# Kernel tuning notes

Measured on AMD Instinct MI355X. Metric: run time of the kernel, lower is better.

The kernel has to match this reference:

```python
import jax, jax.numpy as jnp
import numpy as np

B, C, H, W = 4, 256, 64, 64
NHEAD = 8
KH = KW = 3          # partition = [3, 3] -> 9-token windows, stride 1, padding 1
EPS = 1e-5           # torch LayerNorm default


def setup_inputs() -> dict:
    key = jax.random.key(0)
    ks = jax.random.split(key, 3)
    s = 1.0 / np.sqrt(C)  # xavier-ish scale
    return {
        "src": jax.random.normal(ks[0], (B, C, H, W), jnp.float32),
        "ln_w": jnp.ones((C,), jnp.float32),
        "ln_b": jnp.zeros((C,), jnp.float32),
        "in_proj_w": jax.random.normal(ks[1], (3 * C, C), jnp.float32) * s,
        "in_proj_b": jnp.zeros((3 * C,), jnp.float32),
        "out_proj_w": jax.random.normal(ks[2], (C, C), jnp.float32) * s,
        "out_proj_b": jnp.zeros((C,), jnp.float32),
    }


def reference(src, ln_w, ln_b, in_proj_w, in_proj_b, out_proj_w, out_proj_b):
    b, c, h, w = src.shape
    L = h * w
    S = KH * KW  # 9 tokens per local window
    # --- Unfold: overlapping 3x3 windows, padding 1, stride 1 (torch.nn.Unfold order: c major, kernel pos minor)
    xp = jnp.pad(src, ((0, 0), (0, 0), (1, 1), (1, 1)))
    patches = jnp.stack(
        [xp[:, :, i : i + h, j : j + w] for i in range(KH) for j in range(KW)], axis=2
    )  # [b, c, 9, h, w]
    x = patches.reshape(b, c, S, L).transpose(2, 0, 3, 1).reshape(S, b * L, c)  # [S, bL, c]
    # --- Pre-norm (norm1); note: pos embed in the source is overwritten (q = k = src2), FFN is dead code
    mu = x.mean(-1, keepdims=True)
    var = ((x - mu) ** 2).mean(-1, keepdims=True)
    x2 = (x - mu) / jnp.sqrt(var + EPS) * ln_w + ln_b
    # --- MultiheadAttention (self-attn, eval mode -> no dropout)
    qkv = jnp.einsum("sbc,dc->sbd", x2, in_proj_w) + in_proj_b  # [S, bL, 3c]
    q, k, v = jnp.split(qkv, 3, axis=-1)
    dh = c // NHEAD
    scale = dh ** -0.5
    q = q.reshape(S, b * L, NHEAD, dh) * scale
    k = k.reshape(S, b * L, NHEAD, dh)
    v = v.reshape(S, b * L, NHEAD, dh)
    scores = jnp.einsum("sbhd,tbhd->bhst", q, k)        # [bL, H, 9, 9]
    attn = jax.nn.softmax(scores, axis=-1)
    o = jnp.einsum("bhst,tbhd->sbhd", attn, v).reshape(S, b * L, c)
    o = jnp.einsum("sbc,dc->sbd", o, out_proj_w) + out_proj_b
    y = x + o  # residual
    # --- Fold back (kernel 1x1, stride 1): each output pixel = its window's center token
    center = y[S // 2]  # [bL, c]
    return center.reshape(b, L, c).transpose(0, 2, 1).reshape(b, c, h, w)
```

## Files before the change

### kernel.cpp

```cpp
#include <hip/hip_runtime.h>
#include <math.h>


#define NPIX 16384
#define HW   4096
#define CDIM 256

typedef short  bf16x8 __attribute__((ext_vector_type(8)));
typedef float  f32x4  __attribute__((ext_vector_type(4)));
typedef unsigned short u16x8 __attribute__((ext_vector_type(8)));
typedef unsigned short u16x4 __attribute__((ext_vector_type(4)));

__device__ inline float bf2f(unsigned short u) {
    unsigned v = ((unsigned)u) << 16;
    return __builtin_bit_cast(float, v);
}
__device__ inline unsigned short f2bf(float f) {
    unsigned u = __builtin_bit_cast(unsigned, f);
    u += 0x7FFFu + ((u >> 16) & 1u);
    return (unsigned short)(u >> 16);
}
__device__ inline void sb0() { __builtin_amdgcn_sched_barrier(0); }

__global__ __launch_bounds__(256) void k_prep(const float* __restrict__ Wqkv,
                                              const float* __restrict__ Wout,
                                              const float* __restrict__ bqkv,
                                              const float* __restrict__ lnb,
                                              unsigned short* __restrict__ Wqkvbf,
                                              unsigned short* __restrict__ Woutbf,
                                              float* __restrict__ pads) {
    int bid = blockIdx.x, t = threadIdx.x;
    if (bid < 192) {
        int i = bid * 256 + t;
        float4 v = ((const float4*)Wqkv)[i];
        u16x4 o = { f2bf(v.x), f2bf(v.y), f2bf(v.z), f2bf(v.w) };
        *(u16x4*)(Wqkvbf + i * 4) = o;
    } else if (bid < 256) {
        int i = (bid - 192) * 256 + t;
        float4 v = ((const float4*)Wout)[i];
        u16x4 o = { f2bf(v.x), f2bf(v.y), f2bf(v.z), f2bf(v.w) };
        *(u16x4*)(Woutbf + i * 4) = o;
    } else {
        int tg = (bid - 256) * 256 + t;
        int d = tg >> 4, part = tg & 15;
        int row = 256 + d;
        const float* wr = Wqkv + (size_t)row * CDIM + part * 16;
        float s = 0.f;
        #pragma unroll
        for (int c = 0; c < 16; ++c) s += lnb[part * 16 + c] * wr[c];
        s += __shfl_xor(s, 1);
        s += __shfl_xor(s, 2);
        s += __shfl_xor(s, 4);
        s += __shfl_xor(s, 8);
        if (part == 0) pads[d] = s + bqkv[row];
    }
}

__device__ inline void stage32(const unsigned short* __restrict__ g, int grow0,
                               int koff, unsigned short* dst, int lane) {
    int r16  = lane >> 2;
    int slot = lane & 3;
    #pragma unroll
    for (int it = 0; it < 4; ++it) {
        int row = it * 16 + r16;
        const unsigned short* src = g + (size_t)(grow0 + row) * 256 + koff
                                      + ((slot ^ ((row >> 1) & 3)) * 8);
        __builtin_amdgcn_global_load_lds(
            (const __attribute__((address_space(1))) void*)src,
            (__attribute__((address_space(3))) void*)(dst + it * 16 * 32),
            16, 0, 0);
    }
}

__global__ __launch_bounds__(256, 3) void k_ln_qkv(const float* __restrict__ src,
                                                   const float* __restrict__ lnw,
                                                   const float* __restrict__ lnb,
                                                   const unsigned short* __restrict__ Wbf,
                                                   const float* __restrict__ bias,
                                                   unsigned short* __restrict__ qkvbf) {
    __shared__ unsigned short As[32 * 256];
    __shared__ unsigned short Bs[4 * 4096];
    __shared__ float redS[8 * 33 * 2 + 64];

    int t = threadIdx.x;
    int bid = blockIdx.x;
    int sb = (bid & 7) * 64 + (bid >> 3);
    int n0 = sb * 32;
    int b = n0 >> 12, p0 = n0 & 4095;
    int lane = t & 63, wv = t >> 6;
    int lr = lane & 15, lg = lane >> 4;
    unsigned short* BsW = Bs + wv * 4096;

    stage32(Wbf, wv * 64, 0, BsW, lane);

    float bj[3][4];
    #pragma unroll
    for (int p = 0; p < 3; ++p)
        #pragma unroll
        for (int j = 0; j < 4; ++j)
            bj[p][j] = bias[p * 256 + wv * 64 + j * 16 + lr];

    {
        float* red  = redS;
        float* red2 = redS + 264;
        float* muv  = redS + 528;
        float* rsv  = redS + 560;
        int pix = t & 31, q = t >> 5;
        const float* sp = src + ((size_t)b * CDIM) * HW + p0 + pix;
        float x[32];
        float sum = 0.f, sq = 0.f;
        #pragma unroll
        for (int i = 0; i < 32; ++i) {
            x[i] = sp[(size_t)(q * 32 + i) * HW];
            sum += x[i]; sq += x[i] * x[i];
        }
        red[q * 33 + pix] = sum; red2[q * 33 + pix] = sq;
        __syncthreads();
        if (t < 32) {
            float s = 0.f, s2 = 0.f;
            #pragma unroll
            for (int qq = 0; qq < 8; ++qq) { s += red[qq * 33 + t]; s2 += red2[qq * 33 + t]; }
            float mu = s * (1.f / 256.f);
            float var = fmaxf(s2 * (1.f / 256.f) - mu * mu, 0.f);
            muv[t] = mu; rsv[t] = rsqrtf(var + 1e-5f);
        }
        __syncthreads();
        float mu = muv[pix], rs = rsv[pix];
        #pragma unroll
        for (int c8 = 0; c8 < 4; ++c8) {
            u16x8 o8;
            #pragma unroll
            for (int j = 0; j < 8; ++j) {
                int c = q * 32 + c8 * 8 + j;
                float xn = (x[c8 * 8 + j] - mu) * rs * lnw[c] + lnb[c];
                o8[j] = f2bf(xn);
            }
            int chunk = q * 4 + c8;
            *(u16x8*)((char*)As + (pix * 512 + (((chunk & 7) ^ (pix & 7)) | (chunk & 24)) * 16)) = o8;
        }
    }
    __syncthreads();

    for (int pass = 0; pass < 3; ++pass) {
        int d0 = pass * 256;
        f32x4 acc[2][4] = {};
        #pragma unroll
        for (int kc = 0; kc < 8; ++kc) {
            sb0();
            if (kc < 7) {
                stage32(Wbf, d0 + wv * 64, (kc + 1) * 32,
                        BsW + ((kc + 1) & 1) * 2048, lane);
                asm volatile("s_waitcnt vmcnt(4)" ::: "memory");
            } else if (pass < 2) {
                stage32(Wbf, (pass + 1) * 256 + wv * 64, 0, BsW, lane);
                asm volatile("s_waitcnt vmcnt(4)" ::: "memory");
            } else {
                asm volatile("s_waitcnt vmcnt(0)" ::: "memory");
            }
            sb0();
            const unsigned short* B = BsW + (kc & 1) * 2048;
            int chA = kc * 4 + lg;
            bf16x8 a[2], bb[4];
            #pragma unroll
            for (int i = 0; i < 2; ++i) {
                int r = i * 16 + lr;
                int sl = ((chA & 7) ^ (r & 7)) | (chA & 24);
                a[i] = *(bf16x8*)((char*)As + (r * 512 + sl * 16));
            }
            #pragma unroll
            for (int j = 0; j < 4; ++j) {
                int rb = j * 16 + lr;
                int sl = lg ^ ((rb >> 1) & 3);
                bb[j] = *(bf16x8*)(B + rb * 32 + sl * 8);
            }
            __builtin_amdgcn_s_setprio(1);
            #pragma unroll
            for (int i = 0; i < 2; ++i)
                #pragma unroll
                for (int j = 0; j < 4; ++j)
                    acc[i][j] = __builtin_amdgcn_mfma_f32_16x16x32_bf16(
                        a[i], bb[j], acc[i][j], 0, 0, 0);
            __builtin_amdgcn_s_setprio(0);
        }
        sb0();
        unsigned short* Ct = BsW + 2048;
        #pragma unroll
        for (int j = 0; j < 4; ++j) {
            #pragma unroll
            for (int i = 0; i < 2; ++i)
                #pragma unroll
                for (int r2 = 0; r2 < 4; ++r2) {
                    int row = i * 16 + lg * 4 + r2;
                    int col = j * 16 + lr;
                    int ch  = col >> 3;
                    int sl  = ch ^ (row & 7);
                    Ct[row * 64 + sl * 8 + (col & 7)] = f2bf(acc[i][j][r2] + bj[pass][j]);
                }
        }
        #pragma unroll
        for (int it2 = 0; it2 < 4; ++it2) {
            int row = 8 * it2 + (lane >> 3);
            int chunk = lane & 7;
            int sl = chunk ^ (row & 7);
            bf16x8 v = *(bf16x8*)(Ct + row * 64 + sl * 8);
            *(bf16x8*)(qkvbf + (size_t)(n0 + row) * 768 + d0 + wv * 64 + chunk * 8) = v;
        }
    }
}

__global__ __launch_bounds__(256, 3) void k_attn_proj(const unsigned short* __restrict__ qkvbf,
                                                      const float* __restrict__ pads,
                                                      const unsigned short* __restrict__ Wbf,
                                                      const float* __restrict__ bias,
                                                      const float* __restrict__ src,
                                                      float* __restrict__ out) {
    __shared__ unsigned short Bt[32 * 264];
    __shared__ unsigned short Ws[4 * 4096];
    int t  = threadIdx.x;
    int bid = blockIdx.x;
    int sb  = (bid & 7) * 64 + (bid >> 3);
    int n0 = sb * 32;
    int b  = n0 >> 12;
    int p0 = n0 & 4095;
    int lane = t & 63, wv = t >> 6;
    int lr = lane & 15, lg = lane >> 4;
    unsigned short* WsW = Ws + wv * 4096;

    stage32(Wbf, wv * 64, 0, WsW, lane);

    float bd[4][4];
    #pragma unroll
    for (int i = 0; i < 4; ++i)
        #pragma unroll
        for (int r2 = 0; r2 < 4; ++r2)
            bd[i][r2] = bias[wv * 64 + i * 16 + lg * 4 + r2];

    {
        int pix = t >> 3, h = t & 7;
        int n = n0 + pix;
        int p = n & 4095, hh0 = p >> 6, ww0 = p & 63;
        const float scale = 0.1767766952966369f;

        float qv[32];
        const unsigned short* qp = qkvbf + (size_t)n * 768 + h * 32;
        #pragma unroll
        for (int c8 = 0; c8 < 4; ++c8) {
            bf16x8 v = *(const bf16x8*)(qp + c8 * 8);
            #pragma unroll
            for (int j = 0; j < 8; ++j) qv[c8 * 8 + j] = bf2f((unsigned short)v[j]) * scale;
        }
        float sc[9];
        #pragma unroll
        for (int t9 = 0; t9 < 9; ++t9) {
            int dy = t9 / 3 - 1, dx = t9 % 3 - 1;
            int hh = hh0 + dy, ww = ww0 + dx;
            bool ok = ((unsigned)hh < 64u) && ((unsigned)ww < 64u);
            float a = 0.f;
            if (ok) {
                const unsigned short* kp = qkvbf + (size_t)(n + dy * 64 + dx) * 768 + 256 + h * 32;
                #pragma unroll
                for (int c8 = 0; c8 < 4; ++c8) {
                    bf16x8 v = *(const bf16x8*)(kp + c8 * 8);
                    #pragma unroll
                    for (int j = 0; j < 8; ++j) a += qv[c8 * 8 + j] * bf2f((unsigned short)v[j]);
                }
            } else {
                const float* pk = pads + h * 32;
                #pragma unroll
                for (int j = 0; j < 32; ++j) a += qv[j] * pk[j];
            }
            sc[t9] = a;
        }
        float m = sc[0];
        #pragma unroll
        for (int t9 = 1; t9 < 9; ++t9) m = fmaxf(m, sc[t9]);
        float s = 0.f;
        #pragma unroll
        for (int t9 = 0; t9 < 9; ++t9) { sc[t9] = __expf(sc[t9] - m); s += sc[t9]; }
        float inv = 1.0f / s;

        float ov[32];
        #pragma unroll
        for (int j = 0; j < 32; ++j) ov[j] = 0.f;
        #pragma unroll
        for (int t9 = 0; t9 < 9; ++t9) {
            int dy = t9 / 3 - 1, dx = t9 % 3 - 1;
            int hh = hh0 + dy, ww = ww0 + dx;
            bool ok = ((unsigned)hh < 64u) && ((unsigned)ww < 64u);
            float w = sc[t9] * inv;
            if (ok) {
                const unsigned short* vp = qkvbf + (size_t)(n + dy * 64 + dx) * 768 + 512 + h * 32;
                #pragma unroll
                for (int c8 = 0; c8 < 4; ++c8) {
                    bf16x8 v = *(const bf16x8*)(vp + c8 * 8);
                    #pragma unroll
                    for (int j = 0; j < 8; ++j) ov[c8 * 8 + j] += w * bf2f((unsigned short)v[j]);
                }
            } else {
                const float* pv = pads + 256 + h * 32;
                #pragma unroll
                for (int j = 0; j < 32; ++j) ov[j] += w * pv[j];
            }
        }
        #pragma unroll
        for (int c8 = 0; c8 < 4; ++c8) {
            u16x8 o8;
            #pragma unroll
            for (int j = 0; j < 8; ++j) o8[j] = f2bf(ov[c8 * 8 + j]);
            *(u16x8*)(Bt + pix * 264 + h * 32 + c8 * 8) = o8;
        }
    }
    __syncthreads();

    f32x4 acc[4][2] = {};
    #pragma unroll
    for (int kc = 0; kc < 8; ++kc) {
        sb0();
        if (kc < 7) {
            stage32(Wbf, wv * 64, (kc + 1) * 32, WsW + ((kc + 1) & 1) * 2048, lane);
            asm volatile("s_waitcnt vmcnt(4)" ::: "memory");
        } else {
            asm volatile("s_waitcnt vmcnt(0)" ::: "memory");
        }
        sb0();
        const unsigned short* A = WsW + (kc & 1) * 2048;
        bf16x8 a[4], bb[2];
        #pragma unroll
        for (int i = 0; i < 4; ++i) {
            int ri = i * 16 + lr;
            int sl = lg ^ ((ri >> 1) & 3);
            a[i] = *(bf16x8*)(A + ri * 32 + sl * 8);
        }
        #pragma unroll
        for (int j = 0; j < 2; ++j)
            bb[j] = *(bf16x8*)(Bt + (j * 16 + lr) * 264 + kc * 32 + lg * 8);
        __builtin_amdgcn_s_setprio(1);
        #pragma unroll
        for (int i = 0; i < 4; ++i)
            #pragma unroll
            for (int j = 0; j < 2; ++j)
                acc[i][j] = __builtin_amdgcn_mfma_f32_16x16x32_bf16(
                    a[i], bb[j], acc[i][j], 0, 0, 0);
        __builtin_amdgcn_s_setprio(0);
    }
    #pragma unroll
    for (int i = 0; i < 4; ++i) {
        #pragma unroll
        for (int r2 = 0; r2 < 4; ++r2) {
            int dg = wv * 64 + i * 16 + lg * 4 + r2;
            #pragma unroll
            for (int j = 0; j < 2; ++j) {
                int ng = p0 + j * 16 + lr;
                size_t idx = ((size_t)(b * CDIM + dg)) * HW + ng;
                out[idx] = acc[i][j][r2] + bd[i][r2] + src[idx];
            }
        }
    }
}

extern "C" void kernel_launch(void* const* d_in, const int* in_sizes, int n_in,
                              void* d_out, int out_size, void* d_ws, size_t ws_size,
                              hipStream_t stream) {
    const float* src  = (const float*)d_in[0];
    const float* lnw  = (const float*)d_in[1];
    const float* lnb  = (const float*)d_in[2];
    const float* Wqkv = (const float*)d_in[3];
    const float* bqkv = (const float*)d_in[4];
    const float* Wout = (const float*)d_in[5];
    const float* bout = (const float*)d_in[6];
    float* out = (float*)d_out;

    unsigned short* qkvbf  = (unsigned short*)d_ws;
    unsigned short* Wqkvbf = qkvbf + (size_t)NPIX * 768;
    unsigned short* Woutbf = Wqkvbf + 768 * 256;
    float* pads = (float*)(Woutbf + 256 * 256);

    k_prep<<<288, 256, 0, stream>>>(Wqkv, Wout, bqkv, lnb, Wqkvbf, Woutbf, pads);
    k_ln_qkv<<<512, 256, 0, stream>>>(src, lnw, lnb, Wqkvbf, bqkv, qkvbf);
    k_attn_proj<<<512, 256, 0, stream>>>(qkvbf, pads, Woutbf, bout, src, out);
}
```

Measured before the change: 51.25 us.

## Fuse weight prep into LN+QKV kernel, converting fp32 weights to bf16 on the fly

Removes the separate k_prep launch. The QKV GEMM now reads fp32 Wqkv directly, converts it to bf16 with v_cvt_pk_bf16_f32 and stores it into a single-buffered LDS tile. The Wout conversion and the pads bias dot products move into spare waves of the LN+QKV kernel. This saves one kernel launch and the bf16 weight round-trip through memory. In exchange it drops the async global_load_lds double-buffer pipelining, doubles the global weight bytes each block reads, and lowers launch bounds occupancy from 3 to 2.

```diff
diff --git a/kernel.cpp b/kernel.cpp
--- a/kernel.cpp
+++ b/kernel.cpp
@@ -10,6 +10,7 @@
 typedef float  f32x4  __attribute__((ext_vector_type(4)));
 typedef unsigned short u16x8 __attribute__((ext_vector_type(8)));
 typedef unsigned short u16x4 __attribute__((ext_vector_type(4)));
+typedef unsigned int   u32x4 __attribute__((ext_vector_type(4)));
 
 __device__ inline float bf2f(unsigned short u) {
     unsigned v = ((unsigned)u) << 16;
@@ -21,39 +22,10 @@
     return (unsigned short)(u >> 16);
 }
 __device__ inline void sb0() { __builtin_amdgcn_sched_barrier(0); }
-
-__global__ __launch_bounds__(256) void k_prep(const float* __restrict__ Wqkv,
-                                              const float* __restrict__ Wout,
-                                              const float* __restrict__ bqkv,
-                                              const float* __restrict__ lnb,
-                                              unsigned short* __restrict__ Wqkvbf,
-                                              unsigned short* __restrict__ Woutbf,
-                                              float* __restrict__ pads) {
-    int bid = blockIdx.x, t = threadIdx.x;
-    if (bid < 192) {
-        int i = bid * 256 + t;
-        float4 v = ((const float4*)Wqkv)[i];
-        u16x4 o = { f2bf(v.x), f2bf(v.y), f2bf(v.z), f2bf(v.w) };
-        *(u16x4*)(Wqkvbf + i * 4) = o;
-    } else if (bid < 256) {
-        int i = (bid - 192) * 256 + t;
-        float4 v = ((const float4*)Wout)[i];
-        u16x4 o = { f2bf(v.x), f2bf(v.y), f2bf(v.z), f2bf(v.w) };
-        *(u16x4*)(Woutbf + i * 4) = o;
-    } else {
-        int tg = (bid - 256) * 256 + t;
-        int d = tg >> 4, part = tg & 15;
-        int row = 256 + d;
-        const float* wr = Wqkv + (size_t)row * CDIM + part * 16;
-        float s = 0.f;
-        #pragma unroll
-        for (int c = 0; c < 16; ++c) s += lnb[part * 16 + c] * wr[c];
-        s += __shfl_xor(s, 1);
-        s += __shfl_xor(s, 2);
-        s += __shfl_xor(s, 4);
-        s += __shfl_xor(s, 8);
-        if (part == 0) pads[d] = s + bqkv[row];
-    }
+__device__ inline unsigned cvtpk(float a, float b) {
+    unsigned r;
+    asm("v_cvt_pk_bf16_f32 %0, %1, %2" : "=v"(r) : "v"(a), "v"(b));
+    return r;
 }
 
 __device__ inline void stage32(const unsigned short* __restrict__ g, int grow0,
@@ -72,14 +44,17 @@
     }
 }
 
-__global__ __launch_bounds__(256, 3) void k_ln_qkv(const float* __restrict__ src,
+__global__ __launch_bounds__(256, 2) void k_ln_qkv(const float* __restrict__ src,
                                                    const float* __restrict__ lnw,
                                                    const float* __restrict__ lnb,
-                                                   const unsigned short* __restrict__ Wbf,
-                                                   const float* __restrict__ bias,
-                                                   unsigned short* __restrict__ qkvbf) {
+                                                   const float* __restrict__ Wqkv,
+                                                   const float* __restrict__ bqkv,
+                                                   const float* __restrict__ Wout,
+                                                   unsigned short* __restrict__ qkvbf,
+                                                   unsigned short* __restrict__ Woutbf,
+                                                   float* __restrict__ pads) {
     __shared__ unsigned short As[32 * 256];
-    __shared__ unsigned short Bs[4 * 4096];
+    __shared__ unsigned short Bs[4 * 2048];
     __shared__ float redS[8 * 33 * 2 + 64];
 
     int t = threadIdx.x;
@@ -89,16 +64,14 @@
     int b = n0 >> 12, p0 = n0 & 4095;
     int lane = t & 63, wv = t >> 6;
     int lr = lane & 15, lg = lane >> 4;
-    unsigned short* BsW = Bs + wv * 4096;
-
-    stage32(Wbf, wv * 64, 0, BsW, lane);
+    unsigned short* BsW = Bs + wv * 2048;
 
     float bj[3][4];
     #pragma unroll
     for (int p = 0; p < 3; ++p)
         #pragma unroll
         for (int j = 0; j < 4; ++j)
-            bj[p][j] = bias[p * 256 + wv * 64 + j * 16 + lr];
+            bj[p][j] = bqkv[p * 256 + wv * 64 + j * 16 + lr];
 
     {
         float* red  = redS;
@@ -141,24 +114,41 @@
     }
     __syncthreads();
 
+    if (wv == 2 && lane < 32) {
+        int i = bid * 32 + lane;
+        float4 v = ((const float4*)Wout)[i];
+        u16x4 o = { f2bf(v.x), f2bf(v.y), f2bf(v.z), f2bf(v.w) };
+        *(u16x4*)(Woutbf + i * 4) = o;
+    }
+    if (wv == 3) {
+        int row = 256 + bid;
+        float4 w4 = *(const float4*)(Wqkv + (size_t)row * 256 + lane * 4);
+        float4 l4 = *(const float4*)(lnb + lane * 4);
+        float s = w4.x * l4.x + w4.y * l4.y + w4.z * l4.z + w4.w * l4.w;
+        s += __shfl_xor(s, 1);  s += __shfl_xor(s, 2);  s += __shfl_xor(s, 4);
+        s += __shfl_xor(s, 8);  s += __shfl_xor(s, 16); s += __shfl_xor(s, 32);
+        if (lane == 0) pads[bid] = s + bqkv[row];
+    }
+
+    int rrow = lane >> 2;
+    int kp   = lane & 3;
     for (int pass = 0; pass < 3; ++pass) {
         int d0 = pass * 256;
         f32x4 acc[2][4] = {};
         #pragma unroll
         for (int kc = 0; kc < 8; ++kc) {
-            sb0();
-            if (kc < 7) {
-                stage32(Wbf, d0 + wv * 64, (kc + 1) * 32,
-                        BsW + ((kc + 1) & 1) * 2048, lane);
-                asm volatile("s_waitcnt vmcnt(4)" ::: "memory");
-            } else if (pass < 2) {
-                stage32(Wbf, (pass + 1) * 256 + wv * 64, 0, BsW, lane);
-                asm volatile("s_waitcnt vmcnt(4)" ::: "memory");
-            } else {
-                asm volatile("s_waitcnt vmcnt(0)" ::: "memory");
-            }
-            sb0();
-            const unsigned short* B = BsW + (kc & 1) * 2048;
+            #pragma unroll
+            for (int it = 0; it < 4; ++it) {
+                int r = it * 16 + rrow;
+                const float* gp = Wqkv + (size_t)(d0 + wv * 64 + r) * 256
+                                       + kc * 32 + kp * 8;
+                float4 v0 = *(const float4*)gp;
+                float4 v1 = *(const float4*)(gp + 4);
+                u32x4 o = { cvtpk(v0.x, v0.y), cvtpk(v0.z, v0.w),
+                            cvtpk(v1.x, v1.y), cvtpk(v1.z, v1.w) };
+                int slot = kp ^ ((r >> 1) & 3);
+                *(u32x4*)(BsW + r * 32 + slot * 8) = o;
+            }
             int chA = kc * 4 + lg;
             bf16x8 a[2], bb[4];
             #pragma unroll
@@ -171,19 +161,16 @@
             for (int j = 0; j < 4; ++j) {
                 int rb = j * 16 + lr;
                 int sl = lg ^ ((rb >> 1) & 3);
-                bb[j] = *(bf16x8*)(B + rb * 32 + sl * 8);
-            }
-            __builtin_amdgcn_s_setprio(1);
+                bb[j] = *(bf16x8*)(BsW + rb * 32 + sl * 8);
+            }
             #pragma unroll
             for (int i = 0; i < 2; ++i)
                 #pragma unroll
                 for (int j = 0; j < 4; ++j)
                     acc[i][j] = __builtin_amdgcn_mfma_f32_16x16x32_bf16(
                         a[i], bb[j], acc[i][j], 0, 0, 0);
-            __builtin_amdgcn_s_setprio(0);
-        }
-        sb0();
-        unsigned short* Ct = BsW + 2048;
+        }
+        unsigned short* Ct = BsW;
         #pragma unroll
         for (int j = 0; j < 4; ++j) {
             #pragma unroll
@@ -371,11 +358,10 @@
     float* out = (float*)d_out;
 
     unsigned short* qkvbf  = (unsigned short*)d_ws;
-    unsigned short* Wqkvbf = qkvbf + (size_t)NPIX * 768;
-    unsigned short* Woutbf = Wqkvbf + 768 * 256;
+    unsigned short* Woutbf = qkvbf + (size_t)NPIX * 768;
     float* pads = (float*)(Woutbf + 256 * 256);
 
-    k_prep<<<288, 256, 0, stream>>>(Wqkv, Wout, bqkv, lnb, Wqkvbf, Woutbf, pads);
-    k_ln_qkv<<<512, 256, 0, stream>>>(src, lnw, lnb, Wqkvbf, bqkv, qkvbf);
+    k_ln_qkv<<<512, 256, 0, stream>>>(src, lnw, lnb, Wqkv, bqkv, Wout,
+                                      qkvbf, Woutbf, pads);
     k_attn_proj<<<512, 256, 0, stream>>>(qkvbf, pads, Woutbf, bout, src, out);
 }
```

After: 64.79 us. 1.26x slower.

## Use 8 waves per block in LN+QKV kernel with triple-buffered weight staging

Applied to the files above, without the earlier changes.

The LayerNorm+QKV GEMM kernel now runs with 512 threads (8 waves), each wave owning 32 output columns instead of 64. Weight tiles are staged into a 3-slot ring buffer two k-steps ahead across pass boundaries, replacing the previous double buffer. The aim is more waves to hide memory latency and deeper prefetch. The cost is fewer MFMAs per wave per load and the same A-tile LDS reads duplicated across more waves.

```diff
diff --git a/kernel.cpp b/kernel.cpp
--- a/kernel.cpp
+++ b/kernel.cpp
@@ -56,6 +56,160 @@
     }
 }
 
+__device__ inline void stage32x32(const unsigned short* __restrict__ g, int grow0,
+                                  int koff, unsigned short* dst, int lane) {
+    int rin  = lane >> 2;
+    int slot = lane & 3;
+    #pragma unroll
+    for (int it = 0; it < 2; ++it) {
+        int row = it * 16 + rin;
+        const unsigned short* src = g + (size_t)(grow0 + row) * 256 + koff
+                                      + ((slot ^ ((row >> 1) & 3)) * 8);
+        __builtin_amdgcn_global_load_lds(
+            (const __attribute__((address_space(1))) void*)src,
+            (__attribute__((address_space(3))) void*)(dst + it * 512),
+            16, 0, 0);
+    }
+}
+
+__global__ __launch_bounds__(512, 4) void k_ln_qkv(const float* __restrict__ src,
+                                                   const float* __restrict__ lnw,
+                                                   const float* __restrict__ lnb,
+                                                   const unsigned short* __restrict__ Wbf,
+                                                   const float* __restrict__ bias,
+                                                   unsigned short* __restrict__ qkvbf) {
+    __shared__ unsigned short As[32 * 256];
+    __shared__ unsigned short Ws[8 * 3 * 1024];
+    __shared__ float redS[16 * 33 * 2 + 64];
+
+    int t = threadIdx.x;
+    int bid = blockIdx.x;
+    int sb = (bid & 7) * 64 + (bid >> 3);
+    int n0 = sb * 32;
+    int b = n0 >> 12, p0 = n0 & 4095;
+    int lane = t & 63, wv = t >> 6;
+    int lr = lane & 15, lg = lane >> 4;
+    unsigned short* WsW = Ws + wv * 3072;
+
+    stage32x32(Wbf, wv * 32, 0, WsW, lane);
+    stage32x32(Wbf, wv * 32, 32, WsW + 1024, lane);
+
+    float bj[3][2];
+    #pragma unroll
+    for (int p = 0; p < 3; ++p)
+        #pragma unroll
+        for (int j = 0; j < 2; ++j)
+            bj[p][j] = bias[p * 256 + wv * 32 + j * 16 + lr];
+
+    {
+        float* red  = redS;
+        float* red2 = redS + 528;
+        float* muv  = redS + 1056;
+        float* rsv  = redS + 1088;
+        int pix = t & 31, q = t >> 5;
+        const float* sp = src + ((size_t)b * CDIM) * HW + p0 + pix;
+        float x[16];
+        float sum = 0.f, sq = 0.f;
+        #pragma unroll
+        for (int i = 0; i < 16; ++i) {
+            x[i] = sp[(size_t)(q * 16 + i) * HW];
+            sum += x[i]; sq += x[i] * x[i];
+        }
+        red[q * 33 + pix] = sum; red2[q * 33 + pix] = sq;
+        __syncthreads();
+        if (t < 32) {
+            float s = 0.f, s2 = 0.f;
+            #pragma unroll
+            for (int qq = 0; qq < 16; ++qq) { s += red[qq * 33 + t]; s2 += red2[qq * 33 + t]; }
+            float mu = s * (1.f / 256.f);
+            float var = fmaxf(s2 * (1.f / 256.f) - mu * mu, 0.f);
+            muv[t] = mu; rsv[t] = rsqrtf(var + 1e-5f);
+        }
+        __syncthreads();
+        float mu = muv[pix], rs = rsv[pix];
+        #pragma unroll
+        for (int c8 = 0; c8 < 2; ++c8) {
+            u16x8 o8;
+            #pragma unroll
+            for (int j = 0; j < 8; ++j) {
+                int c = q * 16 + c8 * 8 + j;
+                float xn = (x[c8 * 8 + j] - mu) * rs * lnw[c] + lnb[c];
+                o8[j] = f2bf(xn);
+            }
+            int chunk = q * 2 + c8;
+            *(u16x8*)((char*)As + (pix * 512 + (((chunk & 7) ^ (pix & 7)) | (chunk & 24)) * 16)) = o8;
+        }
+    }
+    __syncthreads();
+
+    for (int pass = 0; pass < 3; ++pass) {
+        int d0 = pass * 256;
+        f32x4 acc[2][2] = {};
+        #pragma unroll
+        for (int kc = 0; kc < 8; ++kc) {
+            int g = pass * 8 + kc;
+            sb0();
+            if (g < 22) {
+                int ng = g + 2;
+                stage32x32(Wbf, (ng >> 3) * 256 + wv * 32, (ng & 7) * 32,
+                           WsW + (ng % 3) * 1024, lane);
+                asm volatile("s_waitcnt vmcnt(4)" ::: "memory");
+            } else if (g == 22) {
+                asm volatile("s_waitcnt vmcnt(2)" ::: "memory");
+            } else {
+                asm volatile("s_waitcnt vmcnt(0)" ::: "memory");
+            }
+            sb0();
+            const unsigned short* B = WsW + (g % 3) * 1024;
+            int chA = kc * 4 + lg;
+            bf16x8 a[2], bb[2];
+            #pragma unroll
+            for (int i = 0; i < 2; ++i) {
+                int r = i * 16 + lr;
+                int sl = ((chA & 7) ^ (r & 7)) | (chA & 24);
+                a[i] = *(bf16x8*)((char*)As + (r * 512 + sl * 16));
+            }
+            #pragma unroll
+            for (int j = 0; j < 2; ++j) {
+                int rb = j * 16 + lr;
+                int sl = lg ^ ((rb >> 1) & 3);
+                bb[j] = *(bf16x8*)(B + rb * 32 + sl * 8);
+            }
+            __builtin_amdgcn_s_setprio(1);
+            #pragma unroll
+            for (int i = 0; i < 2; ++i)
+                #pragma unroll
+                for (int j = 0; j < 2; ++j)
+                    acc[i][j] = __builtin_amdgcn_mfma_f32_16x16x32_bf16(
+                        a[i], bb[j], acc[i][j], 0, 0, 0);
+            __builtin_amdgcn_s_setprio(0);
+        }
+        sb0();
+        unsigned short* Ct = WsW + ((pass * 8 + 7) % 3) * 1024;
+        #pragma unroll
+        for (int j = 0; j < 2; ++j) {
+            #pragma unroll
+            for (int i = 0; i < 2; ++i)
+                #pragma unroll
+                for (int r2 = 0; r2 < 4; ++r2) {
+                    int row = i * 16 + lg * 4 + r2;
+                    int col = j * 16 + lr;
+                    int ch  = col >> 3;
+                    int sl  = ch ^ ((row >> 1) & 3);
+                    Ct[row * 32 + sl * 8 + (col & 7)] = f2bf(acc[i][j][r2] + bj[pass][j]);
+                }
+        }
+        #pragma unroll
+        for (int it2 = 0; it2 < 2; ++it2) {
+            int row = it2 * 16 + (lane >> 2);
+            int chunk = lane & 3;
+            int sl = chunk ^ ((row >> 1) & 3);
+            bf16x8 v = *(bf16x8*)(Ct + row * 32 + sl * 8);
+            *(bf16x8*)(qkvbf + (size_t)(n0 + row) * 768 + d0 + wv * 32 + chunk * 8) = v;
+        }
+    }
+}
+
 __device__ inline void stage32(const unsigned short* __restrict__ g, int grow0,
                                int koff, unsigned short* dst, int lane) {
     int r16  = lane >> 2;
@@ -69,142 +223,6 @@
             (const __attribute__((address_space(1))) void*)src,
             (__attribute__((address_space(3))) void*)(dst + it * 16 * 32),
             16, 0, 0);
-    }
-}
-
-__global__ __launch_bounds__(256, 3) void k_ln_qkv(const float* __restrict__ src,
-                                                   const float* __restrict__ lnw,
-                                                   const float* __restrict__ lnb,
-                                                   const unsigned short* __restrict__ Wbf,
-                                                   const float* __restrict__ bias,
-                                                   unsigned short* __restrict__ qkvbf) {
-    __shared__ unsigned short As[32 * 256];
-    __shared__ unsigned short Bs[4 * 4096];
-    __shared__ float redS[8 * 33 * 2 + 64];
-
-    int t = threadIdx.x;
-    int bid = blockIdx.x;
-    int sb = (bid & 7) * 64 + (bid >> 3);
-    int n0 = sb * 32;
-    int b = n0 >> 12, p0 = n0 & 4095;
-    int lane = t & 63, wv = t >> 6;
-    int lr = lane & 15, lg = lane >> 4;
-    unsigned short* BsW = Bs + wv * 4096;
-
-    stage32(Wbf, wv * 64, 0, BsW, lane);
-
-    float bj[3][4];
-    #pragma unroll
-    for (int p = 0; p < 3; ++p)
-        #pragma unroll
-        for (int j = 0; j < 4; ++j)
-            bj[p][j] = bias[p * 256 + wv * 64 + j * 16 + lr];
-
-    {
-        float* red  = redS;
-        float* red2 = redS + 264;
-        float* muv  = redS + 528;
-        float* rsv  = redS + 560;
-        int pix = t & 31, q = t >> 5;
-        const float* sp = src + ((size_t)b * CDIM) * HW + p0 + pix;
-        float x[32];
-        float sum = 0.f, sq = 0.f;
-        #pragma unroll
-        for (int i = 0; i < 32; ++i) {
-            x[i] = sp[(size_t)(q * 32 + i) * HW];
-            sum += x[i]; sq += x[i] * x[i];
-        }
-        red[q * 33 + pix] = sum; red2[q * 33 + pix] = sq;
-        __syncthreads();
-        if (t < 32) {
-            float s = 0.f, s2 = 0.f;
-            #pragma unroll
-            for (int qq = 0; qq < 8; ++qq) { s += red[qq * 33 + t]; s2 += red2[qq * 33 + t]; }
-            float mu = s * (1.f / 256.f);
-            float var = fmaxf(s2 * (1.f / 256.f) - mu * mu, 0.f);
-            muv[t] = mu; rsv[t] = rsqrtf(var + 1e-5f);
-        }
-        __syncthreads();
-        float mu = muv[pix], rs = rsv[pix];
-        #pragma unroll
-        for (int c8 = 0; c8 < 4; ++c8) {
-            u16x8 o8;
-            #pragma unroll
-            for (int j = 0; j < 8; ++j) {
-                int c = q * 32 + c8 * 8 + j;
-                float xn = (x[c8 * 8 + j] - mu) * rs * lnw[c] + lnb[c];
-                o8[j] = f2bf(xn);
-            }
-            int chunk = q * 4 + c8;
-            *(u16x8*)((char*)As + (pix * 512 + (((chunk & 7) ^ (pix & 7)) | (chunk & 24)) * 16)) = o8;
-        }
-    }
-    __syncthreads();
-
-    for (int pass = 0; pass < 3; ++pass) {
-        int d0 = pass * 256;
-        f32x4 acc[2][4] = {};
-        #pragma unroll
-        for (int kc = 0; kc < 8; ++kc) {
-            sb0();
-            if (kc < 7) {
-                stage32(Wbf, d0 + wv * 64, (kc + 1) * 32,
-                        BsW + ((kc + 1) & 1) * 2048, lane);
-                asm volatile("s_waitcnt vmcnt(4)" ::: "memory");
-            } else if (pass < 2) {
-                stage32(Wbf, (pass + 1) * 256 + wv * 64, 0, BsW, lane);
-                asm volatile("s_waitcnt vmcnt(4)" ::: "memory");
-            } else {
-                asm volatile("s_waitcnt vmcnt(0)" ::: "memory");
-            }
-            sb0();
-            const unsigned short* B = BsW + (kc & 1) * 2048;
-            int chA = kc * 4 + lg;
-            bf16x8 a[2], bb[4];
-            #pragma unroll
-            for (int i = 0; i < 2; ++i) {
-                int r = i * 16 + lr;
-                int sl = ((chA & 7) ^ (r & 7)) | (chA & 24);
-                a[i] = *(bf16x8*)((char*)As + (r * 512 + sl * 16));
-            }
-            #pragma unroll
-            for (int j = 0; j < 4; ++j) {
-                int rb = j * 16 + lr;
-                int sl = lg ^ ((rb >> 1) & 3);
-                bb[j] = *(bf16x8*)(B + rb * 32 + sl * 8);
-            }
-            __builtin_amdgcn_s_setprio(1);
-            #pragma unroll
-            for (int i = 0; i < 2; ++i)
-                #pragma unroll
-                for (int j = 0; j < 4; ++j)
-                    acc[i][j] = __builtin_amdgcn_mfma_f32_16x16x32_bf16(
-                        a[i], bb[j], acc[i][j], 0, 0, 0);
-            __builtin_amdgcn_s_setprio(0);
-        }
-        sb0();
-        unsigned short* Ct = BsW + 2048;
-        #pragma unroll
-        for (int j = 0; j < 4; ++j) {
-            #pragma unroll
-            for (int i = 0; i < 2; ++i)
-                #pragma unroll
-                for (int r2 = 0; r2 < 4; ++r2) {
-                    int row = i * 16 + lg * 4 + r2;
-                    int col = j * 16 + lr;
-                    int ch  = col >> 3;
-                    int sl  = ch ^ (row & 7);
-                    Ct[row * 64 + sl * 8 + (col & 7)] = f2bf(acc[i][j][r2] + bj[pass][j]);
-                }
-        }
-        #pragma unroll
-        for (int it2 = 0; it2 < 4; ++it2) {
-            int row = 8 * it2 + (lane >> 3);
-            int chunk = lane & 7;
-            int sl = chunk ^ (row & 7);
-            bf16x8 v = *(bf16x8*)(Ct + row * 64 + sl * 8);
-            *(bf16x8*)(qkvbf + (size_t)(n0 + row) * 768 + d0 + wv * 64 + chunk * 8) = v;
-        }
     }
 }
 
@@ -376,6 +394,6 @@
     float* pads = (float*)(Woutbf + 256 * 256);
 
     k_prep<<<288, 256, 0, stream>>>(Wqkv, Wout, bqkv, lnb, Wqkvbf, Woutbf, pads);
-    k_ln_qkv<<<512, 256, 0, stream>>>(src, lnw, lnb, Wqkvbf, bqkv, qkvbf);
+    k_ln_qkv<<<512, 512, 0, stream>>>(src, lnw, lnb, Wqkvbf, bqkv, qkvbf);
     k_attn_proj<<<512, 256, 0, stream>>>(qkvbf, pads, Woutbf, bout, src, out);
 }
```

Result: faster. 49.48 us (median of 2 runs) (-3.4%).
